# Kernel tuning notes

Hardware: AMD Instinct MI355X
Metric: run time of the kernel (lower is better)

The kernel has to match this reference:

```python
import jax, jax.numpy as jnp
import numpy as np

B, T, E, H = 2, 256, 256, 4
LN_EPS = 1e-5
W_SCALE = 0.05  # keep softmax logits in a sane range


def _heads(x):
    # [B,T,E*H] -> [B,T,E,H]; torch chunk(H,-1)+stack(-1) puts EH index h*E+d at [...,d,h]
    b, t, eh = x.shape
    return jnp.swapaxes(x.reshape(b, t, H, eh // H), -1, -2)


def setup_inputs() -> dict:
    key = jax.random.key(0)
    k = jax.random.split(key, 6)
    return {
        "position_embeddings": jax.random.normal(k[0], (B, T, E), dtype=jnp.float32),
        "values": jax.random.normal(k[1], (B, T, E), dtype=jnp.float32),
        "ln_w": jnp.ones((E,), dtype=jnp.float32),
        "ln_b": jnp.zeros((E,), dtype=jnp.float32),
        "Wq": jax.random.normal(k[2], (E * H, E), dtype=jnp.float32) * W_SCALE,
        "Wk": jax.random.normal(k[3], (E * H, E), dtype=jnp.float32) * W_SCALE,
        "Wv": jax.random.normal(k[4], (E * H, E), dtype=jnp.float32) * W_SCALE,
        "Wp": jax.random.normal(k[5], (E, E * H), dtype=jnp.float32) * W_SCALE,
    }


def reference(position_embeddings, values, ln_w, ln_b, Wq, Wk, Wv, Wp):
    # LayerNorm over last dim
    mu = jnp.mean(position_embeddings, axis=-1, keepdims=True)
    var = jnp.var(position_embeddings, axis=-1, keepdims=True)
    x = (position_embeddings - mu) * jax.lax.rsqrt(var + LN_EPS) * ln_w + ln_b

    Qh = _heads(x @ Wq.T)        # [B,T,E,H]
    Kh = _heads(x @ Wk.T)        # [B,T,E,H]
    Vh = _heads(values @ Wv.T)   # [B,T,E,H]

    # elementwise Q-K difference: [B,T(query t),T(key w),E,H]
    S = Qh[:, :, None, :, :] - Kh[:, None, :, :, :]
    A = jax.nn.softmax(S, axis=2)  # softmax over w (dim -3)

    # outputs[b,t,d,h] = V[b,t,d,h] * sum_w A[b,t,w,d,h]
    out = jnp.einsum('btdh,btwdh->btdh', Vh, A)

    # flatten(-2): [B,T,E,H] -> [B,T,E*H] with index d*H+h, then project
    return out.reshape(B, T, E * H) @ Wp.T
```

## Files before the change

### kernel.cpp

```cpp
#include <hip/hip_runtime.h>


constexpr int E  = 256;
constexpr int H  = 4;
constexpr int EH = E * H;
constexpr int BT = 512;

__global__ __launch_bounds__(1024) void build_m_kernel(
    const float* __restrict__ Wv, const float* __restrict__ Wp,
    float* __restrict__ MT)
{
    const int tid = threadIdx.x;
    const int jq  = tid & 63;
    const int j0  = jq * 4;
    const int w   = (tid >> 6) & 3;
    const int skc = tid >> 8;
    const int i0  = blockIdx.x * 4;
    const int dB  = blockIdx.y * 64;

    __shared__ float sWp[4][256];
    sWp[tid >> 8][tid & 255] = Wp[(i0 + (tid >> 8)) * EH + blockIdx.y * 256 + (tid & 255)];
    __syncthreads();

    float4 acc = make_float4(0.f, 0.f, 0.f, 0.f);
    #pragma unroll
    for (int h = 0; h < H; ++h) {
        const float* __restrict__ p = Wv + (h * E + dB + skc * 16) * E + j0;
        #pragma unroll
        for (int dd = 0; dd < 16; ++dd) {
            const float4 wv = *(const float4*)(p + dd * E);
            const float  wp = sWp[w][(skc * 16 + dd) * 4 + h];
            acc.x += wp * wv.x; acc.y += wp * wv.y;
            acc.z += wp * wv.z; acc.w += wp * wv.w;
        }
    }

    __shared__ float sAcc[4][4][256];
    *(float4*)&sAcc[skc][w][j0] = acc;
    __syncthreads();

    const int j2 = tid >> 2;
    const int ii = tid & 3;
    float v = sAcc[0][ii][j2] + sAcc[1][ii][j2] + sAcc[2][ii][j2] + sAcc[3][ii][j2];
    atomicAdd(&MT[j2 * E + i0 + ii], v);
}

__global__ __launch_bounds__(1024) void apply_kernel(
    const float* __restrict__ values, const float* __restrict__ MT,
    float* __restrict__ out)
{
    const int tid = threadIdx.x;
    const int eq  = tid & 63;
    const int e0  = eq * 4;
    const int rr  = (tid >> 6) & 1;
    const int jc  = tid >> 7;
    const int r0  = blockIdx.x * 2;

    __shared__ float sv[2][256];
    if (tid < 2 * E) sv[tid >> 8][tid & 255] = values[r0 * E + tid];
    __syncthreads();

    float4 acc = make_float4(0.f, 0.f, 0.f, 0.f);
    #pragma unroll
    for (int jj = 0; jj < 32; ++jj) {
        const int    j = jc * 32 + jj;
        const float4 m = *(const float4*)&MT[j * E + e0];
        const float  s = sv[rr][j];
        acc.x += s * m.x; acc.y += s * m.y; acc.z += s * m.z; acc.w += s * m.w;
    }

    __shared__ float sAcc[8][2][256];
    *(float4*)&sAcc[jc][rr][e0] = acc;
    __syncthreads();

    if (tid < 2 * E) {
        const int r_idx = tid >> 8, e = tid & 255;
        float v = 0.f;
        #pragma unroll
        for (int c = 0; c < 8; ++c) v += sAcc[c][r_idx][e];
        out[(r0 + r_idx) * E + e] = v;
    }
}

extern "C" void kernel_launch(void* const* d_in, const int* in_sizes, int n_in,
                              void* d_out, int out_size, void* d_ws, size_t ws_size,
                              hipStream_t stream) {
    const float* values = (const float*)d_in[1];
    const float* Wv     = (const float*)d_in[6];
    const float* Wp     = (const float*)d_in[7];
    float*       out    = (float*)d_out;
    float*       MT     = (float*)d_ws;

    hipMemsetAsync(MT, 0, E * E * sizeof(float), stream);
    build_m_kernel<<<dim3(64, 4), 1024, 0, stream>>>(Wv, Wp, MT);
    apply_kernel<<<BT / 2, 1024, 0, stream>>>(values, MT, out);
}
```

Baseline: 86.87 us.

## Fuse memset, build and apply stages into one cooperative kernel

Replaces the memset plus two separate kernel launches with a single cooperative kernel of 256 blocks. It zeroes the MT workspace in-kernel, then builds MT with atomics, then applies it to the values, with grid-wide syncs between the phases. The aim is to remove launch and inter-kernel gap overhead. The cost is two grid barriers, and it requires all 256 blocks of 1024 threads to be co-resident.

```diff
diff --git a/kernel.cpp b/kernel.cpp
--- a/kernel.cpp
+++ b/kernel.cpp
@@ -1,84 +1,97 @@
 #include <hip/hip_runtime.h>
+#include <hip/hip_cooperative_groups.h>
+
+namespace cg = cooperative_groups;
 
 
 constexpr int E  = 256;
 constexpr int H  = 4;
 constexpr int EH = E * H;
-constexpr int BT = 512;
 
-__global__ __launch_bounds__(1024) void build_m_kernel(
-    const float* __restrict__ Wv, const float* __restrict__ Wp,
-    float* __restrict__ MT)
-{
-    const int tid = threadIdx.x;
-    const int jq  = tid & 63;
-    const int j0  = jq * 4;
-    const int w   = (tid >> 6) & 3;
-    const int skc = tid >> 8;
-    const int i0  = blockIdx.x * 4;
-    const int dB  = blockIdx.y * 64;
-
-    __shared__ float sWp[4][256];
-    sWp[tid >> 8][tid & 255] = Wp[(i0 + (tid >> 8)) * EH + blockIdx.y * 256 + (tid & 255)];
-    __syncthreads();
-
-    float4 acc = make_float4(0.f, 0.f, 0.f, 0.f);
-    #pragma unroll
-    for (int h = 0; h < H; ++h) {
-        const float* __restrict__ p = Wv + (h * E + dB + skc * 16) * E + j0;
-        #pragma unroll
-        for (int dd = 0; dd < 16; ++dd) {
-            const float4 wv = *(const float4*)(p + dd * E);
-            const float  wp = sWp[w][(skc * 16 + dd) * 4 + h];
-            acc.x += wp * wv.x; acc.y += wp * wv.y;
-            acc.z += wp * wv.z; acc.w += wp * wv.w;
-        }
-    }
-
-    __shared__ float sAcc[4][4][256];
-    *(float4*)&sAcc[skc][w][j0] = acc;
-    __syncthreads();
-
-    const int j2 = tid >> 2;
-    const int ii = tid & 3;
-    float v = sAcc[0][ii][j2] + sAcc[1][ii][j2] + sAcc[2][ii][j2] + sAcc[3][ii][j2];
-    atomicAdd(&MT[j2 * E + i0 + ii], v);
-}
-
-__global__ __launch_bounds__(1024) void apply_kernel(
-    const float* __restrict__ values, const float* __restrict__ MT,
+__global__ __launch_bounds__(1024) void fused_kernel(
+    const float* __restrict__ values, const float* __restrict__ Wv,
+    const float* __restrict__ Wp, float* __restrict__ MT,
     float* __restrict__ out)
 {
+    cg::grid_group grid = cg::this_grid();
     const int tid = threadIdx.x;
-    const int eq  = tid & 63;
-    const int e0  = eq * 4;
-    const int rr  = (tid >> 6) & 1;
-    const int jc  = tid >> 7;
-    const int r0  = blockIdx.x * 2;
+    const int b   = blockIdx.x;
 
-    __shared__ float sv[2][256];
-    if (tid < 2 * E) sv[tid >> 8][tid & 255] = values[r0 * E + tid];
-    __syncthreads();
+    __shared__ float sWp [4][256];
+    __shared__ float sAcc[4][4][256];
+    __shared__ float sv  [2][256];
+    __shared__ float sAc2[8][2][256];
 
-    float4 acc = make_float4(0.f, 0.f, 0.f, 0.f);
-    #pragma unroll
-    for (int jj = 0; jj < 32; ++jj) {
-        const int    j = jc * 32 + jj;
-        const float4 m = *(const float4*)&MT[j * E + e0];
-        const float  s = sv[rr][j];
-        acc.x += s * m.x; acc.y += s * m.y; acc.z += s * m.z; acc.w += s * m.w;
+    {
+        const int idx = b * 1024 + tid;
+        if (idx < E * E) MT[idx] = 0.f;
     }
+    grid.sync();
 
-    __shared__ float sAcc[8][2][256];
-    *(float4*)&sAcc[jc][rr][e0] = acc;
-    __syncthreads();
+    {
+        const int i0 = (b >> 2) * 4;
+        const int dB = (b & 3) * 64;
+        const int jq = tid & 63, j0 = jq * 4;
+        const int w  = (tid >> 6) & 3;
+        const int skc = tid >> 8;
 
-    if (tid < 2 * E) {
-        const int r_idx = tid >> 8, e = tid & 255;
-        float v = 0.f;
+        sWp[tid >> 8][tid & 255] = Wp[(i0 + (tid >> 8)) * EH + (b & 3) * 256 + (tid & 255)];
+        __syncthreads();
+
+        float4 acc = make_float4(0.f, 0.f, 0.f, 0.f);
         #pragma unroll
-        for (int c = 0; c < 8; ++c) v += sAcc[c][r_idx][e];
-        out[(r0 + r_idx) * E + e] = v;
+        for (int h = 0; h < H; ++h) {
+            const float* __restrict__ p = Wv + (h * E + dB + skc * 16) * E + j0;
+            #pragma unroll
+            for (int dd = 0; dd < 16; ++dd) {
+                const float4 wv = *(const float4*)(p + dd * E);
+                const float  wp = sWp[w][(skc * 16 + dd) * 4 + h];
+                acc.x += wp * wv.x; acc.y += wp * wv.y;
+                acc.z += wp * wv.z; acc.w += wp * wv.w;
+            }
+        }
+
+        *(float4*)&sAcc[skc][w][j0] = acc;
+        __syncthreads();
+
+        const int j2 = tid >> 2;
+        const int ii = tid & 3;
+        const float v = sAcc[0][ii][j2] + sAcc[1][ii][j2]
+                      + sAcc[2][ii][j2] + sAcc[3][ii][j2];
+        atomicAdd(&MT[j2 * E + i0 + ii], v);
+    }
+    __threadfence();
+    grid.sync();
+
+    {
+        const int r0 = b * 2;
+        const int eq = tid & 63, e0 = eq * 4;
+        const int rr = (tid >> 6) & 1;
+        const int jc = tid >> 7;
+
+        if (tid < 2 * E) sv[tid >> 8][tid & 255] = values[r0 * E + tid];
+        __syncthreads();
+
+        float4 acc = make_float4(0.f, 0.f, 0.f, 0.f);
+        #pragma unroll
+        for (int jj = 0; jj < 32; ++jj) {
+            const int    j = jc * 32 + jj;
+            const float4 m = *(const float4*)&MT[j * E + e0];
+            const float  s = sv[rr][j];
+            acc.x += s * m.x; acc.y += s * m.y;
+            acc.z += s * m.z; acc.w += s * m.w;
+        }
+
+        *(float4*)&sAc2[jc][rr][e0] = acc;
+        __syncthreads();
+
+        if (tid < 2 * E) {
+            const int r_idx = tid >> 8, e = tid & 255;
+            float v = 0.f;
+            #pragma unroll
+            for (int c = 0; c < 8; ++c) v += sAc2[c][r_idx][e];
+            out[(r0 + r_idx) * E + e] = v;
+        }
     }
 }
 
@@ -91,7 +104,7 @@
     float*       out    = (float*)d_out;
     float*       MT     = (float*)d_ws;
 
-    hipMemsetAsync(MT, 0, E * E * sizeof(float), stream);
-    build_m_kernel<<<dim3(64, 4), 1024, 0, stream>>>(Wv, Wp, MT);
-    apply_kernel<<<BT / 2, 1024, 0, stream>>>(values, MT, out);
+    void* args[] = { (void*)&values, (void*)&Wv, (void*)&Wp, (void*)&MT, (void*)&out };
+    hipLaunchCooperativeKernel((const void*)fused_kernel,
+                               dim3(256), dim3(1024), args, 0, stream);
 }
```

New measurement: 208.6 us. +140.1%, slower.
